# Kernel optimization log

Measured on AMD Instinct MI355X. Metric: run time of the kernel, lower is better.

Reference implementation:

```python
import jax, jax.numpy as jnp
import numpy as np

B, S, EMB, HEAD = 8, 2048, 2048, 128
ROPE_BASE = 10000.0


def _rope(x):
    # x: [B, S, D]; standard rotate-half rotary position embedding
    d = x.shape[-1]
    half = d // 2
    inv_freq = 1.0 / (ROPE_BASE ** (jnp.arange(half, dtype=jnp.float32) / half))  # [half]
    ang = jnp.arange(x.shape[-2], dtype=jnp.float32)[:, None] * inv_freq           # [S, half]
    cos, sin = jnp.cos(ang), jnp.sin(ang)
    x1, x2 = x[..., :half], x[..., half:]
    return jnp.concatenate([x1 * cos - x2 * sin, x1 * sin + x2 * cos], axis=-1)


def setup_inputs() -> dict:
    key = jax.random.key(0)
    ks = jax.random.split(key, 7)
    sc = 1.0 / np.sqrt(EMB)
    return {
        "x": jax.random.normal(ks[0], (B, S, EMB), dtype=jnp.float32),
        "Wq": jax.random.normal(ks[1], (EMB, HEAD), dtype=jnp.float32) * sc,
        "bq": jax.random.normal(ks[2], (HEAD,), dtype=jnp.float32) * 0.02,
        "Wk": jax.random.normal(ks[3], (EMB, HEAD), dtype=jnp.float32) * sc,
        "bk": jax.random.normal(ks[4], (HEAD,), dtype=jnp.float32) * 0.02,
        "Wv": jax.random.normal(ks[5], (EMB, HEAD), dtype=jnp.float32) * sc,
        "bv": jax.random.normal(ks[6], (HEAD,), dtype=jnp.float32) * 0.02,
    }


def reference(x, Wq, bq, Wk, bk, Wv, bv):
    # single-head causal self-attention with RoPE (cache=None path)
    q = _rope(x @ Wq + bq)            # [B, S, HEAD]
    k = _rope(x @ Wk + bk)            # [B, S, HEAD]
    v = x @ Wv + bv                   # [B, S, HEAD]
    scale = 1.0 / jnp.sqrt(jnp.float32(HEAD))
    scores = jnp.einsum('bqd,bkd->bqk', q, k) * scale   # [B, S, S]
    causal = jnp.tril(jnp.ones((S, S), dtype=bool))
    scores = jnp.where(causal, scores, -jnp.inf)
    weights = jax.nn.softmax(scores, axis=-1)
    return jnp.einsum('bqk,bkd->bqd', weights, v)       # [B, S, HEAD]
```

## Files before the change

### kernel.cpp

```cpp
#include <hip/hip_runtime.h>

typedef __bf16 bf16;
typedef __bf16 bf16x8 __attribute__((ext_vector_type(8)));
typedef float f32x4 __attribute__((ext_vector_type(4)));

#define S_LEN 2048
#define EMBD 2048
#define HD 128

__device__ inline void gload16(const void* g, void* l) {
  __builtin_amdgcn_global_load_lds(
      (const __attribute__((address_space(1))) unsigned int*)g,
      (__attribute__((address_space(3))) unsigned int*)l, 16, 0, 0);
}

__global__ __launch_bounds__(256) void k_prep(const float* __restrict__ Wq,
                                              const float* __restrict__ Wk,
                                              const float* __restrict__ Wv,
                                              bf16* __restrict__ wt) {
  __shared__ bf16 wls[64 * 72];

  const int t = threadIdx.x;
  const int bid = blockIdx.x;
  const int mat = bid >> 6;
  const int nt = bid & 1;
  const int kt = (bid & 63) >> 1;
  const int k0 = kt * 64, n0 = nt * 64;
  const float* W = (mat == 0) ? Wq : ((mat == 1) ? Wk : Wv);

#pragma unroll
  for (int i = 0; i < 4; ++i) {
    int e = i * 256 + t;
    int r = e >> 4, c4 = e & 15;
    float4 v = *(const float4*)(W + (size_t)(k0 + r) * HD + n0 + c4 * 4);
    union { bf16 h[4]; uint2 u; } p;
    p.h[0] = (bf16)v.x; p.h[1] = (bf16)v.y;
    p.h[2] = (bf16)v.z; p.h[3] = (bf16)v.w;
    *(uint2*)&wls[r * 72 + c4 * 4] = p.u;
  }
  __syncthreads();
#pragma unroll
  for (int i = 0; i < 2; ++i) {
    int slot = i * 256 + t;
    int n_loc = slot >> 3, kq = slot & 7;
    int n = n0 + n_loc;
    int kbase = (kq * 8) ^ ((n & 7) << 3);
    union { bf16 h[8]; uint4 u; } p;
#pragma unroll
    for (int j = 0; j < 8; ++j) p.h[j] = wls[(kbase + j) * 72 + n_loc];
    *(uint4*)&wt[(size_t)(mat * HD + n) * EMBD + k0 + kq * 8] = p.u;
  }
}

__global__ __launch_bounds__(512, 6) void k_qkv(
    const float* __restrict__ x, const bf16* __restrict__ wt,
    const float* __restrict__ bq, const float* __restrict__ bk,
    const float* __restrict__ bv, bf16* __restrict__ Qw, bf16* __restrict__ Kw,
    bf16* __restrict__ Vtw) {
  __shared__ __align__(16) bf16 xs[2][64 * 72];
  __shared__ __align__(16) bf16 wts[2][128 * 64];

  const int tid = threadIdx.x;
  const int lane = tid & 63;
  const int wave = tid >> 6;
  const int wm = wave >> 2;
  const int wn = wave & 3;
  const int l15 = lane & 15;
  const int lh = lane >> 4;

  const int bid = blockIdx.x;
  const int xcd = bid & 7;
  const int idx = bid >> 3;
  const int by = idx % 3;
  const int mt = xcd * 32 + idx / 3;
  const int row0 = mt * 64;

  f32x4 acc[2][2];
#pragma unroll
  for (int mf = 0; mf < 2; ++mf)
#pragma unroll
    for (int f = 0; f < 2; ++f) acc[mf][f] = {};

  int xr_[2], xk_[2];
  const float* xp_[2];
#pragma unroll
  for (int i = 0; i < 2; ++i) {
    int e = (i * 512 + tid) * 4;
    xr_[i] = e >> 6;
    xk_[i] = e & 63;
    xp_[i] = x + (size_t)(row0 + xr_[i]) * EMBD + xk_[i];
  }
  const bf16* wp_[2];
  int we_[2];
#pragma unroll
  for (int i = 0; i < 2; ++i) {
    int e = (i * 512 + tid) * 8;
    int np = e >> 6, k = e & 63;
    wp_[i] = wt + (size_t)(by * 128 + np) * EMBD + k;
    we_[i] = e;
  }

  auto stage_issue = [&](int ks, int buf, float4* xr) {
#pragma unroll
    for (int i = 0; i < 2; ++i) xr[i] = *(const float4*)(xp_[i] + ks * 64);
#pragma unroll
    for (int i = 0; i < 2; ++i) gload16(wp_[i] + ks * 64, &wts[buf][we_[i]]);
  };
  auto xwrite = [&](int buf, const float4* xr) {
#pragma unroll
    for (int i = 0; i < 2; ++i) {
      union { bf16 h[4]; uint2 u; } p;
      p.h[0] = (bf16)xr[i].x; p.h[1] = (bf16)xr[i].y;
      p.h[2] = (bf16)xr[i].z; p.h[3] = (bf16)xr[i].w;
      *(uint2*)&xs[buf][xr_[i] * 72 + xk_[i]] = p.u;
    }
  };

  {
    float4 xr[2];
    stage_issue(0, 0, xr);
    xwrite(0, xr);
  }
  __syncthreads();

  for (int ks = 0; ks < EMBD / 64; ++ks) {
    const int cur = ks & 1;
    float4 xr[2];
    if (ks + 1 < EMBD / 64) stage_issue(ks + 1, cur ^ 1, xr);

#pragma unroll
    for (int kk = 0; kk < 2; ++kk) {
      bf16x8 a[2];
#pragma unroll
      for (int mf = 0; mf < 2; ++mf)
        a[mf] = *(const bf16x8*)&xs[cur][(wm * 32 + mf * 16 + l15) * 72 + kk * 32 + lh * 8];
      const int klin = (kk * 32 + lh * 8) ^ ((l15 & 7) << 3);
#pragma unroll
      for (int f = 0; f < 2; ++f) {
        int col = f * 64 + wn * 16 + l15;
        bf16x8 b = *(const bf16x8*)&wts[cur][col * 64 + klin];
#pragma unroll
        for (int mf = 0; mf < 2; ++mf)
          acc[mf][f] =
              __builtin_amdgcn_mfma_f32_16x16x32_bf16(a[mf], b, acc[mf][f], 0, 0, 0);
      }
    }

    if (ks + 1 < EMBD / 64) xwrite(cur ^ 1, xr);
    __syncthreads();
  }

  const int bb = row0 >> 11;
  const int s0 = row0 & (S_LEN - 1);

  if (by < 2) {
    const float* bias = (by == 0) ? bq : bk;
    const int colA = wn * 16 + l15;
    const int colB = colA + 64;
    float biasA = bias[colA], biasB = bias[colB];
    float invf = exp2f((float)colA * -0.20762050593046014f);
#pragma unroll
    for (int mf = 0; mf < 2; ++mf) {
#pragma unroll
      for (int r = 0; r < 4; ++r) {
        int s = s0 + wm * 32 + mf * 16 + lh * 4 + r;
        float xa_ = acc[mf][0][r] + biasA;
        float xb_ = acc[mf][1][r] + biasB;
        float sn, cs;
        sincosf((float)s * invf, &sn, &cs);
        float oa = xa_ * cs - xb_ * sn;
        float ob = xa_ * sn + xb_ * cs;
        if (by == 0) {
          Qw[(size_t)(bb * S_LEN + s) * HD + colA] = (bf16)oa;
          Qw[(size_t)(bb * S_LEN + s) * HD + colB] = (bf16)ob;
        } else {
          int sw = (s & 7) << 3;
          Kw[(size_t)(bb * S_LEN + s) * HD + (colA ^ sw)] = (bf16)oa;
          Kw[(size_t)(bb * S_LEN + s) * HD + (colB ^ sw)] = (bf16)ob;
        }
      }
    }
  } else {
    bf16* vstage = &wts[0][0];
#pragma unroll
    for (int f = 0; f < 2; ++f) {
      int dv = f * 64 + wn * 16 + l15;
      float biasV = bv[dv];
#pragma unroll
      for (int mf = 0; mf < 2; ++mf)
#pragma unroll
        for (int r = 0; r < 4; ++r) {
          int mrow = wm * 32 + mf * 16 + lh * 4 + r;
          vstage[dv * 72 + mrow] = (bf16)(acc[mf][f][r] + biasV);
        }
    }
    __syncthreads();
#pragma unroll
    for (int i = 0; i < 2; ++i) {
      int c = i * 512 + tid;
      int dv = c >> 3, kq = c & 7;
      uint4 v = *(const uint4*)&vstage[dv * 72 + kq * 8];
      int slot = (kq * 8) ^ ((dv & 7) << 3);
      *(uint4*)&Vtw[((size_t)(bb * HD + dv) << 11) + s0 + slot] = v;
    }
  }
}

__global__ __launch_bounds__(512) void k_attn(
    const bf16* __restrict__ Qw, const bf16* __restrict__ Kw,
    const bf16* __restrict__ Vtw, float* __restrict__ out) {
  __shared__ __align__(16) char arena[131072];
  __shared__ __align__(16) bf16 pld[8 * 16 * 72];
  __shared__ float mls[64], lls[64];

  bf16(*kls)[64 * 128] = (bf16(*)[64 * 128])arena;
  bf16(*vls)[128 * 64] = (bf16(*)[128 * 64])(arena + 65536);
  float* oml = (float*)arena;

  const int tid = threadIdx.x;
  const int lane = tid & 63;
  const int wave = tid >> 6;
  const int grp = wave >> 2;
  const int w4 = wave & 3;
  const int l15 = lane & 15;
  const int lh = lane >> 4;
  const int t256 = tid & 255;

  const int bid = blockIdx.x;
  const int batch = bid & 7;
  const int qt = 31 - (bid >> 3);
  const int qbase = qt * 64;
  const int nt = qt + 1;
  const int mysteps = (nt - grp + 1) >> 1;
  const int maxst = (nt + 1) >> 1;

  const bf16* kbat = Kw + (size_t)(batch * S_LEN) * HD;
  const bf16* vbat = Vtw + ((size_t)(batch * HD) << 11);

  auto stage = [&](int t, int buf) {
    bf16* kdst = kls[grp * 2 + buf];
    bf16* vdst = vls[grp * 2 + buf];
    const bf16* kbase = kbat + (size_t)(t * 64) * HD;
#pragma unroll
    for (int i = 0; i < 4; ++i) {
      int c = i * 256 + t256;
      gload16(kbase + c * 8, kdst + c * 8);
    }
    const bf16* vbase = vbat + t * 64;
#pragma unroll
    for (int i = 0; i < 4; ++i) {
      int c = i * 256 + t256;
      int dv = c >> 3, kq = (c & 7) * 8;
      gload16(vbase + ((size_t)dv << 11) + kq, vdst + c * 8);
    }
  };

  bf16x8 qa[4];
  {
    const bf16* qptr = Qw + (size_t)(batch * S_LEN + qbase + w4 * 16 + l15) * HD;
#pragma unroll
    for (int kk = 0; kk < 4; ++kk) qa[kk] = *(const bf16x8*)(qptr + kk * 32 + lh * 8);
  }

  f32x4 o[8];
#pragma unroll
  for (int i = 0; i < 8; ++i) o[i] = {};
  float m[4], lsum[4];
#pragma unroll
  for (int r = 0; r < 4; ++r) { m[r] = -__builtin_inff(); lsum[r] = 0.f; }

  const float scale = 0.08838834764831845f;

  if (mysteps > 0) stage(grp, 0);
  __syncthreads();

  for (int i = 0; i < maxst; ++i) {
    if (i + 1 < mysteps) stage(2 * (i + 1) + grp, (i + 1) & 1);
    if (i < mysteps) {
      const int t = 2 * i + grp;
      const int buf = grp * 2 + (i & 1);
      const int kv0 = t * 64;

      f32x4 sc[4];
#pragma unroll
      for (int nf = 0; nf < 4; ++nf) sc[nf] = {};
      __builtin_amdgcn_s_setprio(1);
#pragma unroll
      for (int kk = 0; kk < 4; ++kk) {
#pragma unroll
        for (int nf = 0; nf < 4; ++nf) {
          int row = nf * 16 + l15;
          int dlin = (kk * 32 + lh * 8) ^ ((row & 7) << 3);
          bf16x8 kb = *(const bf16x8*)&kls[buf][row * 128 + dlin];
          sc[nf] = __builtin_amdgcn_mfma_f32_16x16x32_bf16(qa[kk], kb, sc[nf], 0, 0, 0);
        }
      }
      __builtin_amdgcn_s_setprio(0);

      const bool diag = (t == qt);
      const int qg0 = qbase + w4 * 16 + lh * 4;
#pragma unroll
      for (int nf = 0; nf < 4; ++nf) {
        int kvg = kv0 + nf * 16 + l15;
#pragma unroll
        for (int r = 0; r < 4; ++r) {
          float v = sc[nf][r] * scale;
          if (diag && kvg > qg0 + r) v = -__builtin_inff();
          sc[nf][r] = v;
        }
      }

      float mnew[4], alpha[4], rs[4];
#pragma unroll
      for (int r = 0; r < 4; ++r) {
        float v = fmaxf(fmaxf(sc[0][r], sc[1][r]), fmaxf(sc[2][r], sc[3][r]));
#pragma unroll
        for (int sh = 1; sh < 16; sh <<= 1) v = fmaxf(v, __shfl_xor(v, sh));
        mnew[r] = fmaxf(m[r], v);
        alpha[r] = __expf(m[r] - mnew[r]);
        m[r] = mnew[r];
        rs[r] = 0.f;
      }

      bf16* pw = &pld[wave * 16 * 72];
#pragma unroll
      for (int nf = 0; nf < 4; ++nf)
#pragma unroll
        for (int r = 0; r < 4; ++r) {
          float p = __expf(sc[nf][r] - mnew[r]);
          bf16 pb = (bf16)p;
          pw[(lh * 4 + r) * 72 + nf * 16 + l15] = pb;
          rs[r] += (float)pb;
        }
#pragma unroll
      for (int r = 0; r < 4; ++r) {
        float v = rs[r];
#pragma unroll
        for (int sh = 1; sh < 16; sh <<= 1) v += __shfl_xor(v, sh);
        lsum[r] = lsum[r] * alpha[r] + v;
      }
#pragma unroll
      for (int i2 = 0; i2 < 8; ++i2)
#pragma unroll
        for (int r = 0; r < 4; ++r) o[i2][r] *= alpha[r];

      __builtin_amdgcn_s_setprio(1);
#pragma unroll
      for (int kkv = 0; kkv < 2; ++kkv) {
        bf16x8 pa = *(const bf16x8*)&pw[l15 * 72 + kkv * 32 + lh * 8];
#pragma unroll
        for (int df = 0; df < 8; ++df) {
          int dv = df * 16 + l15;
          int klin = (kkv * 32 + lh * 8) ^ ((dv & 7) << 3);
          bf16x8 vb = *(const bf16x8*)&vls[buf][dv * 64 + klin];
          o[df] = __builtin_amdgcn_mfma_f32_16x16x32_bf16(pa, vb, o[df], 0, 0, 0);
        }
      }
      __builtin_amdgcn_s_setprio(0);
    }
    __syncthreads();
  }

  if (grp == 1) {
#pragma unroll
    for (int df = 0; df < 8; ++df)
#pragma unroll
      for (int r = 0; r < 4; ++r)
        oml[(w4 * 16 + lh * 4 + r) * 128 + df * 16 + l15] = o[df][r];
    if (l15 == 0) {
#pragma unroll
      for (int r = 0; r < 4; ++r) {
        mls[w4 * 16 + lh * 4 + r] = m[r];
        lls[w4 * 16 + lh * 4 + r] = lsum[r];
      }
    }
  }
  __syncthreads();
  if (grp == 0) {
#pragma unroll
    for (int r = 0; r < 4; ++r) {
      int row = w4 * 16 + lh * 4 + r;
      float m1 = mls[row], l1 = lls[row];
      float mm = fmaxf(m[r], m1);
      float s0 = __expf(m[r] - mm);
      float s1 = __expf(m1 - mm);
      float inv = 1.0f / (lsum[r] * s0 + l1 * s1);
      float* op = out + (size_t)(batch * S_LEN + qbase + row) * HD;
#pragma unroll
      for (int df = 0; df < 8; ++df)
        op[df * 16 + l15] =
            (o[df][r] * s0 + oml[row * 128 + df * 16 + l15] * s1) * inv;
    }
  }
}

extern "C" void kernel_launch(void* const* d_in, const int* in_sizes, int n_in,
                              void* d_out, int out_size, void* d_ws, size_t ws_size,
                              hipStream_t stream) {
  const float* x = (const float*)d_in[0];
  const float* Wq = (const float*)d_in[1];
  const float* bq = (const float*)d_in[2];
  const float* Wk = (const float*)d_in[3];
  const float* bk = (const float*)d_in[4];
  const float* Wv = (const float*)d_in[5];
  const float* bv = (const float*)d_in[6];
  float* out = (float*)d_out;

  char* ws = (char*)d_ws;
  bf16* wt  = (bf16*)(ws);
  bf16* Qw  = (bf16*)(ws + (size_t)(2u << 20));
  bf16* Kw  = (bf16*)(ws + (size_t)(6u << 20));
  bf16* Vtw = (bf16*)(ws + (size_t)(10u << 20));

  hipLaunchKernelGGL(k_prep, dim3(192), dim3(256), 0, stream, Wq, Wk, Wv, wt);
  hipLaunchKernelGGL(k_qkv, dim3(768), dim3(512), 0, stream, x, wt, bq, bk, bv,
                     Qw, Kw, Vtw);
  hipLaunchKernelGGL(k_attn, dim3(256), dim3(512), 0, stream, Qw, Kw, Vtw, out);
}
```

Before: 100.9 us.

## Deepen QKV projection pipeline with register double-buffering and explicit waitcnt barriers

Restructures the QKV projection GEMM main loop so x loads are issued two stages ahead into alternating register sets, while the weight tiles go straight to LDS one stage ahead. __syncthreads is replaced by hand-placed s_waitcnt vmcnt(2) plus s_barrier, with sched_barriers pinning instruction order. The goal is to hide global-load latency behind MFMA work rather than draining all outstanding loads each iteration. The cost is fragile hand-scheduled code with manually unrolled prologue and epilogue, and an extra sync before the V staging path.

```diff
diff --git a/kernel.cpp b/kernel.cpp
--- a/kernel.cpp
+++ b/kernel.cpp
@@ -100,13 +100,7 @@
     we_[i] = e;
   }
 
-  auto stage_issue = [&](int ks, int buf, float4* xr) {
-#pragma unroll
-    for (int i = 0; i < 2; ++i) xr[i] = *(const float4*)(xp_[i] + ks * 64);
-#pragma unroll
-    for (int i = 0; i < 2; ++i) gload16(wp_[i] + ks * 64, &wts[buf][we_[i]]);
-  };
-  auto xwrite = [&](int buf, const float4* xr) {
+  auto xwr = [&](int buf, const float4* xr) {
 #pragma unroll
     for (int i = 0; i < 2; ++i) {
       union { bf16 h[4]; uint2 u; } p;
@@ -115,40 +109,66 @@
       *(uint2*)&xs[buf][xr_[i] * 72 + xk_[i]] = p.u;
     }
   };
-
-  {
-    float4 xr[2];
-    stage_issue(0, 0, xr);
-    xwrite(0, xr);
-  }
-  __syncthreads();
-
-  for (int ks = 0; ks < EMBD / 64; ++ks) {
-    const int cur = ks & 1;
-    float4 xr[2];
-    if (ks + 1 < EMBD / 64) stage_issue(ks + 1, cur ^ 1, xr);
-
+  auto mfma_phase = [&](int cur) {
+    const bf16* xsc = xs[cur];
+    const bf16* wtc = wts[cur];
 #pragma unroll
     for (int kk = 0; kk < 2; ++kk) {
       bf16x8 a[2];
 #pragma unroll
       for (int mf = 0; mf < 2; ++mf)
-        a[mf] = *(const bf16x8*)&xs[cur][(wm * 32 + mf * 16 + l15) * 72 + kk * 32 + lh * 8];
+        a[mf] = *(const bf16x8*)&xsc[(wm * 32 + mf * 16 + l15) * 72 + kk * 32 + lh * 8];
       const int klin = (kk * 32 + lh * 8) ^ ((l15 & 7) << 3);
 #pragma unroll
       for (int f = 0; f < 2; ++f) {
-        int col = f * 64 + wn * 16 + l15;
-        bf16x8 b = *(const bf16x8*)&wts[cur][col * 64 + klin];
+        bf16x8 b = *(const bf16x8*)&wtc[(f * 64 + wn * 16 + l15) * 64 + klin];
 #pragma unroll
         for (int mf = 0; mf < 2; ++mf)
           acc[mf][f] =
               __builtin_amdgcn_mfma_f32_16x16x32_bf16(a[mf], b, acc[mf][f], 0, 0, 0);
       }
     }
-
-    if (ks + 1 < EMBD / 64) xwrite(cur ^ 1, xr);
-    __syncthreads();
-  }
+  };
+
+  float4 sA[2], sB[2];
+  sA[0] = *(const float4*)(xp_[0]);
+  sA[1] = *(const float4*)(xp_[1]);
+  gload16(wp_[0], &wts[0][we_[0]]);
+  gload16(wp_[1], &wts[0][we_[1]]);
+  xwr(0, sA);
+  sB[0] = *(const float4*)(xp_[0] + 64);
+  sB[1] = *(const float4*)(xp_[1] + 64);
+  asm volatile("s_waitcnt vmcnt(2) lgkmcnt(0)" ::: "memory");
+  __builtin_amdgcn_s_barrier();
+  __builtin_amdgcn_sched_barrier(0);
+
+  auto step = [&](int ks, float4(&ld)[2], float4(&wr)[2]) {
+    gload16(wp_[0] + (ks + 1) * 64, &wts[(ks + 1) & 1][we_[0]]);
+    gload16(wp_[1] + (ks + 1) * 64, &wts[(ks + 1) & 1][we_[1]]);
+    __builtin_amdgcn_sched_barrier(0);
+    ld[0] = *(const float4*)(xp_[0] + (ks + 2) * 64);
+    ld[1] = *(const float4*)(xp_[1] + (ks + 2) * 64);
+    __builtin_amdgcn_sched_barrier(0);
+    mfma_phase(ks & 1);
+    xwr((ks + 1) & 1, wr);
+    asm volatile("s_waitcnt vmcnt(2) lgkmcnt(0)" ::: "memory");
+    __builtin_amdgcn_s_barrier();
+    __builtin_amdgcn_sched_barrier(0);
+  };
+
+  for (int kp = 0; kp < 15; ++kp) {
+    step(2 * kp, sA, sB);
+    step(2 * kp + 1, sB, sA);
+  }
+  gload16(wp_[0] + 31 * 64, &wts[1][we_[0]]);
+  gload16(wp_[1] + 31 * 64, &wts[1][we_[1]]);
+  __builtin_amdgcn_sched_barrier(0);
+  mfma_phase(0);
+  xwr(1, sB);
+  asm volatile("s_waitcnt vmcnt(0) lgkmcnt(0)" ::: "memory");
+  __builtin_amdgcn_s_barrier();
+  __builtin_amdgcn_sched_barrier(0);
+  mfma_phase(1);
 
   const int bb = row0 >> 11;
   const int s0 = row0 & (S_LEN - 1);
@@ -181,6 +201,7 @@
       }
     }
   } else {
+    __syncthreads();
     bf16* vstage = &wts[0][0];
 #pragma unroll
     for (int f = 0; f < 2; ++f) {
```

New measurement: 101.1 us. About the same (+0.2%).

## Fuse V projection into Q/K blocks to cut redundant x reads

Applied to the files above, without the earlier changes.

The QKV projection grid shrinks from three blocks per row tile to two, each computing Q or K plus half of V, so the fp32 input x is loaded and converted twice instead of three times. The x shared tile switches from padded rows to an XOR swizzle, and MFMA sections get raised wave priority. The trade-off is higher per-block register and LDS use, reflected in a lower occupancy hint, and less parallelism across the grid.

```diff
diff --git a/kernel.cpp b/kernel.cpp
--- a/kernel.cpp
+++ b/kernel.cpp
@@ -52,13 +52,13 @@
   }
 }
 
-__global__ __launch_bounds__(512, 6) void k_qkv(
+__global__ __launch_bounds__(512, 4) void k_qkv(
     const float* __restrict__ x, const bf16* __restrict__ wt,
     const float* __restrict__ bq, const float* __restrict__ bk,
     const float* __restrict__ bv, bf16* __restrict__ Qw, bf16* __restrict__ Kw,
     bf16* __restrict__ Vtw) {
-  __shared__ __align__(16) bf16 xs[2][64 * 72];
-  __shared__ __align__(16) bf16 wts[2][128 * 64];
+  __shared__ __align__(16) bf16 xs[2][64 * 64];
+  __shared__ __align__(16) bf16 wts[2][192 * 64];
 
   const int tid = threadIdx.x;
   const int lane = tid & 63;
@@ -69,17 +69,16 @@
   const int lh = lane >> 4;
 
   const int bid = blockIdx.x;
-  const int xcd = bid & 7;
-  const int idx = bid >> 3;
-  const int by = idx % 3;
-  const int mt = xcd * 32 + idx / 3;
+  const int g = bid >> 3;
+  const int by = g & 1;
+  const int mt = (bid & 7) * 32 + (g >> 1);
   const int row0 = mt * 64;
 
-  f32x4 acc[2][2];
+  f32x4 acc[2][3];
 #pragma unroll
   for (int mf = 0; mf < 2; ++mf)
 #pragma unroll
-    for (int f = 0; f < 2; ++f) acc[mf][f] = {};
+    for (int f = 0; f < 3; ++f) acc[mf][f] = {};
 
   int xr_[2], xk_[2];
   const float* xp_[2];
@@ -90,13 +89,14 @@
     xk_[i] = e & 63;
     xp_[i] = x + (size_t)(row0 + xr_[i]) * EMBD + xk_[i];
   }
-  const bf16* wp_[2];
-  int we_[2];
-#pragma unroll
-  for (int i = 0; i < 2; ++i) {
+  const bf16* wp_[3];
+  int we_[3];
+#pragma unroll
+  for (int i = 0; i < 3; ++i) {
     int e = (i * 512 + tid) * 8;
     int np = e >> 6, k = e & 63;
-    wp_[i] = wt + (size_t)(by * 128 + np) * EMBD + k;
+    int ng = (np < 128) ? by * 128 + np : 256 + by * 64 + (np - 128);
+    wp_[i] = wt + (size_t)ng * EMBD + k;
     we_[i] = e;
   }
 
@@ -104,7 +104,7 @@
 #pragma unroll
     for (int i = 0; i < 2; ++i) xr[i] = *(const float4*)(xp_[i] + ks * 64);
 #pragma unroll
-    for (int i = 0; i < 2; ++i) gload16(wp_[i] + ks * 64, &wts[buf][we_[i]]);
+    for (int i = 0; i < 3; ++i) gload16(wp_[i] + ks * 64, &wts[buf][we_[i]]);
   };
   auto xwrite = [&](int buf, const float4* xr) {
 #pragma unroll
@@ -112,7 +112,7 @@
       union { bf16 h[4]; uint2 u; } p;
       p.h[0] = (bf16)xr[i].x; p.h[1] = (bf16)xr[i].y;
       p.h[2] = (bf16)xr[i].z; p.h[3] = (bf16)xr[i].w;
-      *(uint2*)&xs[buf][xr_[i] * 72 + xk_[i]] = p.u;
+      *(uint2*)&xs[buf][xr_[i] * 64 + (xk_[i] ^ ((xr_[i] & 7) << 3))] = p.u;
     }
   };
 
@@ -124,39 +124,43 @@
   __syncthreads();
 
   for (int ks = 0; ks < EMBD / 64; ++ks) {
-    const int cur = ks & 1;
+    const int c = ks & 1, pbuf = c ^ 1;
     float4 xr[2];
-    if (ks + 1 < EMBD / 64) stage_issue(ks + 1, cur ^ 1, xr);
-
+    if (ks < EMBD / 64 - 1) stage_issue(ks + 1, pbuf, xr);
+
+    __builtin_amdgcn_s_setprio(1);
 #pragma unroll
     for (int kk = 0; kk < 2; ++kk) {
       bf16x8 a[2];
 #pragma unroll
-      for (int mf = 0; mf < 2; ++mf)
-        a[mf] = *(const bf16x8*)&xs[cur][(wm * 32 + mf * 16 + l15) * 72 + kk * 32 + lh * 8];
-      const int klin = (kk * 32 + lh * 8) ^ ((l15 & 7) << 3);
-#pragma unroll
-      for (int f = 0; f < 2; ++f) {
-        int col = f * 64 + wn * 16 + l15;
-        bf16x8 b = *(const bf16x8*)&wts[cur][col * 64 + klin];
+      for (int mf = 0; mf < 2; ++mf) {
+        int row = wm * 32 + mf * 16 + l15;
+        a[mf] = *(const bf16x8*)&xs[c][row * 64 + ((kk * 32 + lh * 8) ^ ((row & 7) << 3))];
+      }
+#pragma unroll
+      for (int f = 0; f < 3; ++f) {
+        int col = (f < 2) ? (f * 64 + wn * 16 + l15) : (128 + wn * 16 + l15);
+        int klin = (kk * 32 + lh * 8) ^ ((col & 7) << 3);
+        bf16x8 b = *(const bf16x8*)&wts[c][col * 64 + klin];
 #pragma unroll
         for (int mf = 0; mf < 2; ++mf)
           acc[mf][f] =
               __builtin_amdgcn_mfma_f32_16x16x32_bf16(a[mf], b, acc[mf][f], 0, 0, 0);
       }
     }
-
-    if (ks + 1 < EMBD / 64) xwrite(cur ^ 1, xr);
+    __builtin_amdgcn_s_setprio(0);
+
+    if (ks < EMBD / 64 - 1) xwrite(pbuf, xr);
     __syncthreads();
   }
 
   const int bb = row0 >> 11;
   const int s0 = row0 & (S_LEN - 1);
 
-  if (by < 2) {
-    const float* bias = (by == 0) ? bq : bk;
+  {
     const int colA = wn * 16 + l15;
     const int colB = colA + 64;
+    const float* bias = (by == 0) ? bq : bk;
     float biasA = bias[colA], biasB = bias[colB];
     float invf = exp2f((float)colA * -0.20762050593046014f);
 #pragma unroll
@@ -180,27 +184,24 @@
         }
       }
     }
-  } else {
-    bf16* vstage = &wts[0][0];
-#pragma unroll
-    for (int f = 0; f < 2; ++f) {
-      int dv = f * 64 + wn * 16 + l15;
-      float biasV = bv[dv];
-#pragma unroll
-      for (int mf = 0; mf < 2; ++mf)
-#pragma unroll
-        for (int r = 0; r < 4; ++r) {
-          int mrow = wm * 32 + mf * 16 + lh * 4 + r;
-          vstage[dv * 72 + mrow] = (bf16)(acc[mf][f][r] + biasV);
-        }
-    }
+  }
+  {
+    bf16* vstage = &xs[0][0];
+    const int dvl = wn * 16 + l15;
+    float biasV = bv[by * 64 + dvl];
+#pragma unroll
+    for (int mf = 0; mf < 2; ++mf)
+#pragma unroll
+      for (int r = 0; r < 4; ++r) {
+        int mrow = wm * 32 + mf * 16 + lh * 4 + r;
+        vstage[dvl * 72 + mrow] = (bf16)(acc[mf][2][r] + biasV);
+      }
     __syncthreads();
-#pragma unroll
-    for (int i = 0; i < 2; ++i) {
-      int c = i * 512 + tid;
-      int dv = c >> 3, kq = c & 7;
-      uint4 v = *(const uint4*)&vstage[dv * 72 + kq * 8];
-      int slot = (kq * 8) ^ ((dv & 7) << 3);
+    {
+      int dvl2 = tid >> 3, kq = tid & 7;
+      uint4 v = *(const uint4*)&vstage[dvl2 * 72 + kq * 8];
+      int dv = by * 64 + dvl2;
+      int slot = (kq * 8) ^ ((dvl2 & 7) << 3);
       *(uint4*)&Vtw[((size_t)(bb * HD + dv) << 11) + s0 + slot] = v;
     }
   }
@@ -413,7 +414,7 @@
   bf16* Vtw = (bf16*)(ws + (size_t)(10u << 20));
 
   hipLaunchKernelGGL(k_prep, dim3(192), dim3(256), 0, stream, Wq, Wk, Wv, wt);
-  hipLaunchKernelGGL(k_qkv, dim3(768), dim3(512), 0, stream, x, wt, bq, bk, bv,
+  hipLaunchKernelGGL(k_qkv, dim3(512), dim3(512), 0, stream, x, wt, bq, bk, bv,
                      Qw, Kw, Vtw);
   hipLaunchKernelGGL(k_attn, dim3(256), dim3(512), 0, stream, Qw, Kw, Vtw, out);
 }
```

After: 98.22 us, median of 3. 1.03x faster.
